# Kernel optimization log

Measured on AMD Instinct MI355X. Metric: run time of the kernel, lower is better.

Reference implementation:

```python
import jax, jax.numpy as jnp
import numpy as np
from jax import lax

SOBEL_X = np.array([[1, 0, -1], [2, 0, -2], [1, 0, -1]], dtype=np.float32)
SOBEL_Y = np.array([[1, 2, 1], [0, 0, 0], [-1, -2, -1]], dtype=np.float32)
K_XX = np.array([[1, -2, 1], [2, -4, 2], [1, -2, 1]], dtype=np.float32)
K_YY = np.array([[1, 2, 1], [-2, -4, -2], [1, 2, 1]], dtype=np.float32)
K_XY = np.array([[-1, 0, 1], [0, 0, 0], [1, 0, -1]], dtype=np.float32)
EPS = 1e-6


def _depthwise3x3(x, k2d):
    # x: [B, C, H, W]; k2d: [3, 3] -> depthwise conv, groups = C, padding 1
    C = x.shape[1]
    kernel = jnp.broadcast_to(jnp.asarray(k2d, dtype=x.dtype), (C, 1, 3, 3))
    return lax.conv_general_dilated(
        x, kernel, window_strides=(1, 1), padding=((1, 1), (1, 1)),
        dimension_numbers=("NCHW", "OIHW", "NCHW"), feature_group_count=C)


def setup_inputs() -> dict:
    key = jax.random.key(0)
    x = jax.random.normal(key, (16, 128, 128, 128), dtype=jnp.float32)
    return {"x": x}


def reference(x):
    Gx = _depthwise3x3(x, SOBEL_X)
    Gy = _depthwise3x3(x, SOBEL_Y)
    Ixx = _depthwise3x3(x, K_XX)
    Iyy = _depthwise3x3(x, K_YY)
    Ixy = _depthwise3x3(x, K_XY)

    Gx2 = Gx * Gx
    Gy2 = Gy * Gy
    grad_mag = jnp.sqrt(Gx2 + Gy2 + EPS)
    numerator = Gx2 * Iyy - 2.0 * Gx * Gy * Ixy + Gy2 * Ixx
    denominator = (Gx2 + Gy2 + EPS) ** 1.5
    curvature = numerator / denominator

    attn = jax.nn.softmax(grad_mag + curvature, axis=1) + 1.0  # softmax over channels
    return attn * x
```

## Files before the change

kernel.cpp:

```cpp
#include <hip/hip_runtime.h>


#define GCA_B 16
#define GCA_C 128
#define GCA_H 128
#define GCA_W 128
#define CGRP  16
#define CPW   (GCA_C/CGRP)

__device__ __forceinline__ float gca_score6(float cpl, float cpc, float cpr,
                                            float cml, float cmc, float cmr,
                                            float cyl, float cyc, float cyr) {
    const float Gx  = cpl - cpr;
    const float Gy  = fmaf(2.f, cmc, cml + cmr);
    const float Ixx = fmaf(-2.f, cpc, cpl + cpr);
    const float Ixy = cmr - cml;
    const float Iyy = fmaf(2.f, cyc, cyl + cyr);
    const float gy2 = Gy * Gy;
    const float g2e = fmaf(Gx, Gx, gy2 + 1e-6f);
    const float r   = rsqrtf(g2e);
    const float gm  = g2e * r;
    const float t   = Gx * Iyy;
    const float p   = Gy * Ixy;
    const float inner = fmaf(-2.f, p, t);
    const float q   = gy2 * Ixx;
    const float num = fmaf(Gx, inner, q);
    const float r3  = (r * r) * r;
    return fmaf(num, r3, gm);
}

__global__ __launch_bounds__(512) void gca_fused6(const float* __restrict__ x,
                                                  float* __restrict__ out) {
    const int tx = threadIdx.x;
    const int ty = threadIdx.y;

    const int id  = blockIdx.x;
    const int swz = ((id & 7) << 8) | (id >> 3);
    const int h   = swz & 127;
    const int b   = swz >> 7;

    const int w0 = tx * 4;
    const int c0 = ty * CPW;

    const int hm = (h > 0) ? h - 1 : 0;
    const int hp = (h < GCA_H - 1) ? h + 1 : GCA_H - 1;
    const float mh0 = (h > 0) ? 1.f : 0.f;
    const float mh2 = (h < GCA_H - 1) ? 1.f : 0.f;
    const float mwA = (tx > 0) ? 1.f : 0.f;
    const float mwB = (tx < 31) ? 1.f : 0.f;

    const size_t plane = (size_t)GCA_H * GCA_W;
    const float* base = x   + ((size_t)b * GCA_C + c0) * plane;
    float* obase      = out + ((size_t)b * GCA_C + c0) * plane;

    const int r0off = hm * GCA_W + w0;
    const int r1off = h  * GCA_W + w0;
    const int r2off = hp * GCA_W + w0;

    float4 s[CPW];
    float4 lmax = make_float4(-3.0e38f, -3.0e38f, -3.0e38f, -3.0e38f);

    #pragma unroll
    for (int i = 0; i < CPW; ++i) {
        const float* p = base + (size_t)i * plane;
        float4 v0 = *(const float4*)(p + r0off);
        const float4 v1 = *(const float4*)(p + r1off);
        float4 v2 = *(const float4*)(p + r2off);
        float L0 = __shfl_up(v0.w, 1), R0 = __shfl_down(v0.x, 1);
        const float L1 = __shfl_up(v1.w, 1), R1 = __shfl_down(v1.x, 1);
        float L2 = __shfl_up(v2.w, 1), R2 = __shfl_down(v2.x, 1);

        v0.x *= mh0; v0.y *= mh0; v0.z *= mh0; v0.w *= mh0; L0 *= mh0; R0 *= mh0;
        v2.x *= mh2; v2.y *= mh2; v2.z *= mh2; v2.w *= mh2; L2 *= mh2; R2 *= mh2;

        float cp0, cp1, cp2, cp3, cp4, cp5;
        float cm0, cm1, cm2, cm3, cm4, cm5;
        float cy0, cy1, cy2, cy3, cy4, cy5;

        cp0 = fmaf(2.f, L1, L0 + L2) * mwA;
        cm0 = (L0 - L2) * mwA;
        cy0 = fmaf(-4.f, L1 * mwA, cp0);

        cp1 = fmaf(2.f, v1.x, v0.x + v2.x); cm1 = v0.x - v2.x; cy1 = fmaf(-4.f, v1.x, cp1);
        cp2 = fmaf(2.f, v1.y, v0.y + v2.y); cm2 = v0.y - v2.y; cy2 = fmaf(-4.f, v1.y, cp2);
        cp3 = fmaf(2.f, v1.z, v0.z + v2.z); cm3 = v0.z - v2.z; cy3 = fmaf(-4.f, v1.z, cp3);
        cp4 = fmaf(2.f, v1.w, v0.w + v2.w); cm4 = v0.w - v2.w; cy4 = fmaf(-4.f, v1.w, cp4);

        cp5 = fmaf(2.f, R1, R0 + R2) * mwB;
        cm5 = (R0 - R2) * mwB;
        cy5 = fmaf(-4.f, R1 * mwB, cp5);

        float4 sc;
        sc.x = gca_score6(cp0, cp1, cp2,  cm0, cm1, cm2,  cy0, cy1, cy2);
        sc.y = gca_score6(cp1, cp2, cp3,  cm1, cm2, cm3,  cy1, cy2, cy3);
        sc.z = gca_score6(cp2, cp3, cp4,  cm2, cm3, cm4,  cy2, cy3, cy4);
        sc.w = gca_score6(cp3, cp4, cp5,  cm3, cm4, cm5,  cy3, cy4, cy5);
        s[i] = sc;
        lmax.x = fmaxf(lmax.x, sc.x);
        lmax.y = fmaxf(lmax.y, sc.y);
        lmax.z = fmaxf(lmax.z, sc.z);
        lmax.w = fmaxf(lmax.w, sc.w);
    }

    __shared__ float4 redmax[CGRP][32];
    __shared__ float4 redsum[CGRP][32];

    redmax[ty][tx] = lmax;
    __syncthreads();
    float4 gmax = make_float4(-3.0e38f, -3.0e38f, -3.0e38f, -3.0e38f);
    #pragma unroll
    for (int g = 0; g < CGRP; ++g) {
        const float4 m = redmax[g][tx];
        gmax.x = fmaxf(gmax.x, m.x);
        gmax.y = fmaxf(gmax.y, m.y);
        gmax.z = fmaxf(gmax.z, m.z);
        gmax.w = fmaxf(gmax.w, m.w);
    }

    float4 lsum = make_float4(0.f, 0.f, 0.f, 0.f);
    #pragma unroll
    for (int i = 0; i < CPW; ++i) {
        float4 e;
        e.x = __expf(s[i].x - gmax.x);
        e.y = __expf(s[i].y - gmax.y);
        e.z = __expf(s[i].z - gmax.z);
        e.w = __expf(s[i].w - gmax.w);
        s[i] = e;
        lsum.x += e.x; lsum.y += e.y; lsum.z += e.z; lsum.w += e.w;
    }
    redsum[ty][tx] = lsum;
    __syncthreads();
    float4 tot = make_float4(0.f, 0.f, 0.f, 0.f);
    #pragma unroll
    for (int g = 0; g < CGRP; ++g) {
        const float4 sm = redsum[g][tx];
        tot.x += sm.x; tot.y += sm.y; tot.z += sm.z; tot.w += sm.w;
    }
    const float invx = 1.f / tot.x, invy = 1.f / tot.y;
    const float invz = 1.f / tot.z, invw = 1.f / tot.w;

    #pragma unroll
    for (int i = 0; i < CPW; ++i) {
        const float4 xv = *(const float4*)(base + (size_t)i * plane + r1off);
        float4 o;
        o.x = fmaf(s[i].x * invx, xv.x, xv.x);
        o.y = fmaf(s[i].y * invy, xv.y, xv.y);
        o.z = fmaf(s[i].z * invz, xv.z, xv.z);
        o.w = fmaf(s[i].w * invw, xv.w, xv.w);
        *(float4*)(obase + (size_t)i * plane + r1off) = o;
    }
}

extern "C" void kernel_launch(void* const* d_in, const int* in_sizes, int n_in,
                              void* d_out, int out_size, void* d_ws, size_t ws_size,
                              hipStream_t stream) {
    (void)in_sizes; (void)n_in; (void)d_ws; (void)ws_size; (void)out_size;
    const float* x = (const float*)d_in[0];
    float* out = (float*)d_out;
    dim3 block(32, CGRP, 1);
    dim3 grid(GCA_B * GCA_H, 1, 1);
    gca_fused6<<<grid, block, 0, stream>>>(x, out);
}
```

Baseline: 69.90 us.

## Process two output rows per block to reuse vertical halo loads

Each block now computes two adjacent rows, loading four input rows instead of three per output row, so vertical-neighbour reads are shared between the two outputs. Horizontal neighbours are now obtained by shuffling the vertically combined column sums (six shuffles per row) rather than the raw row values. The grid is halved, and registers per thread roughly double (two score arrays), which may lower occupancy or cause spills under the 512-thread launch bound.

```diff
diff --git a/kernel.cpp b/kernel.cpp
--- a/kernel.cpp
+++ b/kernel.cpp
@@ -8,7 +8,7 @@
 #define CGRP  16
 #define CPW   (GCA_C/CGRP)
 
-__device__ __forceinline__ float gca_score6(float cpl, float cpc, float cpr,
+__device__ __forceinline__ float gca_score8(float cpl, float cpc, float cpr,
                                             float cml, float cmc, float cmr,
                                             float cyl, float cyc, float cyr) {
     const float Gx  = cpl - cpr;
@@ -29,23 +29,55 @@
     return fmaf(num, r3, gm);
 }
 
-__global__ __launch_bounds__(512) void gca_fused6(const float* __restrict__ x,
+#define GCA_ROW_SCORES(vA, vB, vC, scv, lmaxv)                                 \
+    {                                                                          \
+        const float cpA = fmaf(2.f, (vB).x, (vA).x + (vC).x);                  \
+        const float cmA = (vA).x - (vC).x;                                     \
+        const float cyA = fmaf(-4.f, (vB).x, cpA);                             \
+        const float cpB = fmaf(2.f, (vB).y, (vA).y + (vC).y);                  \
+        const float cmB = (vA).y - (vC).y;                                     \
+        const float cyB = fmaf(-4.f, (vB).y, cpB);                             \
+        const float cpC = fmaf(2.f, (vB).z, (vA).z + (vC).z);                  \
+        const float cmC = (vA).z - (vC).z;                                     \
+        const float cyC = fmaf(-4.f, (vB).z, cpC);                             \
+        const float cpD = fmaf(2.f, (vB).w, (vA).w + (vC).w);                  \
+        const float cmD = (vA).w - (vC).w;                                     \
+        const float cyD = fmaf(-4.f, (vB).w, cpD);                             \
+        const float cpL = __shfl_up(cpD, 1) * mwA;                             \
+        const float cmL = __shfl_up(cmD, 1) * mwA;                             \
+        const float cyL = __shfl_up(cyD, 1) * mwA;                             \
+        const float cpR = __shfl_down(cpA, 1) * mwB;                           \
+        const float cmR = __shfl_down(cmA, 1) * mwB;                           \
+        const float cyR = __shfl_down(cyA, 1) * mwB;                           \
+        (scv).x = gca_score8(cpL, cpA, cpB, cmL, cmA, cmB, cyL, cyA, cyB);     \
+        (scv).y = gca_score8(cpA, cpB, cpC, cmA, cmB, cmC, cyA, cyB, cyC);     \
+        (scv).z = gca_score8(cpB, cpC, cpD, cmB, cmC, cmD, cyB, cyC, cyD);     \
+        (scv).w = gca_score8(cpC, cpD, cpR, cmC, cmD, cmR, cyC, cyD, cyR);     \
+        (lmaxv).x = fmaxf((lmaxv).x, (scv).x);                                 \
+        (lmaxv).y = fmaxf((lmaxv).y, (scv).y);                                 \
+        (lmaxv).z = fmaxf((lmaxv).z, (scv).z);                                 \
+        (lmaxv).w = fmaxf((lmaxv).w, (scv).w);                                 \
+    }
+
+__global__ __launch_bounds__(512) void gca_fused8(const float* __restrict__ x,
                                                   float* __restrict__ out) {
     const int tx = threadIdx.x;
     const int ty = threadIdx.y;
 
     const int id  = blockIdx.x;
-    const int swz = ((id & 7) << 8) | (id >> 3);
-    const int h   = swz & 127;
-    const int b   = swz >> 7;
+    const int swz = ((id & 7) << 7) | (id >> 3);
+    const int hq  = swz & 63;
+    const int b   = swz >> 6;
+    const int h0  = hq * 2;
+    const int h1  = h0 + 1;
 
     const int w0 = tx * 4;
     const int c0 = ty * CPW;
 
-    const int hm = (h > 0) ? h - 1 : 0;
-    const int hp = (h < GCA_H - 1) ? h + 1 : GCA_H - 1;
-    const float mh0 = (h > 0) ? 1.f : 0.f;
-    const float mh2 = (h < GCA_H - 1) ? 1.f : 0.f;
+    const int hmm = (h0 > 0) ? h0 - 1 : 0;
+    const int hpp = (h1 < GCA_H - 1) ? h1 + 1 : GCA_H - 1;
+    const float mTop = (h0 > 0) ? 1.f : 0.f;
+    const float mBot = (h1 < GCA_H - 1) ? 1.f : 0.f;
     const float mwA = (tx > 0) ? 1.f : 0.f;
     const float mwB = (tx < 31) ? 1.f : 0.f;
 
@@ -53,101 +85,94 @@
     const float* base = x   + ((size_t)b * GCA_C + c0) * plane;
     float* obase      = out + ((size_t)b * GCA_C + c0) * plane;
 
-    const int r0off = hm * GCA_W + w0;
-    const int r1off = h  * GCA_W + w0;
-    const int r2off = hp * GCA_W + w0;
+    const int offm = hmm * GCA_W + w0;
+    const int off0 = h0  * GCA_W + w0;
+    const int off1 = h1  * GCA_W + w0;
+    const int offp = hpp * GCA_W + w0;
 
-    float4 s[CPW];
-    float4 lmax = make_float4(-3.0e38f, -3.0e38f, -3.0e38f, -3.0e38f);
+    float4 sT[CPW], sB[CPW];
+    float4 lmaxT = make_float4(-3.0e38f, -3.0e38f, -3.0e38f, -3.0e38f);
+    float4 lmaxB = lmaxT;
 
     #pragma unroll
     for (int i = 0; i < CPW; ++i) {
         const float* p = base + (size_t)i * plane;
-        float4 v0 = *(const float4*)(p + r0off);
-        const float4 v1 = *(const float4*)(p + r1off);
-        float4 v2 = *(const float4*)(p + r2off);
-        float L0 = __shfl_up(v0.w, 1), R0 = __shfl_down(v0.x, 1);
-        const float L1 = __shfl_up(v1.w, 1), R1 = __shfl_down(v1.x, 1);
-        float L2 = __shfl_up(v2.w, 1), R2 = __shfl_down(v2.x, 1);
+        float4 vm = *(const float4*)(p + offm);
+        const float4 v0 = *(const float4*)(p + off0);
+        const float4 v1 = *(const float4*)(p + off1);
+        float4 vp = *(const float4*)(p + offp);
+        vm.x *= mTop; vm.y *= mTop; vm.z *= mTop; vm.w *= mTop;
+        vp.x *= mBot; vp.y *= mBot; vp.z *= mBot; vp.w *= mBot;
 
-        v0.x *= mh0; v0.y *= mh0; v0.z *= mh0; v0.w *= mh0; L0 *= mh0; R0 *= mh0;
-        v2.x *= mh2; v2.y *= mh2; v2.z *= mh2; v2.w *= mh2; L2 *= mh2; R2 *= mh2;
-
-        float cp0, cp1, cp2, cp3, cp4, cp5;
-        float cm0, cm1, cm2, cm3, cm4, cm5;
-        float cy0, cy1, cy2, cy3, cy4, cy5;
-
-        cp0 = fmaf(2.f, L1, L0 + L2) * mwA;
-        cm0 = (L0 - L2) * mwA;
-        cy0 = fmaf(-4.f, L1 * mwA, cp0);
-
-        cp1 = fmaf(2.f, v1.x, v0.x + v2.x); cm1 = v0.x - v2.x; cy1 = fmaf(-4.f, v1.x, cp1);
-        cp2 = fmaf(2.f, v1.y, v0.y + v2.y); cm2 = v0.y - v2.y; cy2 = fmaf(-4.f, v1.y, cp2);
-        cp3 = fmaf(2.f, v1.z, v0.z + v2.z); cm3 = v0.z - v2.z; cy3 = fmaf(-4.f, v1.z, cp3);
-        cp4 = fmaf(2.f, v1.w, v0.w + v2.w); cm4 = v0.w - v2.w; cy4 = fmaf(-4.f, v1.w, cp4);
-
-        cp5 = fmaf(2.f, R1, R0 + R2) * mwB;
-        cm5 = (R0 - R2) * mwB;
-        cy5 = fmaf(-4.f, R1 * mwB, cp5);
-
-        float4 sc;
-        sc.x = gca_score6(cp0, cp1, cp2,  cm0, cm1, cm2,  cy0, cy1, cy2);
-        sc.y = gca_score6(cp1, cp2, cp3,  cm1, cm2, cm3,  cy1, cy2, cy3);
-        sc.z = gca_score6(cp2, cp3, cp4,  cm2, cm3, cm4,  cy2, cy3, cy4);
-        sc.w = gca_score6(cp3, cp4, cp5,  cm3, cm4, cm5,  cy3, cy4, cy5);
-        s[i] = sc;
-        lmax.x = fmaxf(lmax.x, sc.x);
-        lmax.y = fmaxf(lmax.y, sc.y);
-        lmax.z = fmaxf(lmax.z, sc.z);
-        lmax.w = fmaxf(lmax.w, sc.w);
+        GCA_ROW_SCORES(vm, v0, v1, sT[i], lmaxT);
+        GCA_ROW_SCORES(v0, v1, vp, sB[i], lmaxB);
     }
 
-    __shared__ float4 redmax[CGRP][32];
-    __shared__ float4 redsum[CGRP][32];
+    __shared__ float4 redmaxT[CGRP][32];
+    __shared__ float4 redmaxB[CGRP][32];
+    __shared__ float4 redsumT[CGRP][32];
+    __shared__ float4 redsumB[CGRP][32];
 
-    redmax[ty][tx] = lmax;
+    redmaxT[ty][tx] = lmaxT;
+    redmaxB[ty][tx] = lmaxB;
     __syncthreads();
-    float4 gmax = make_float4(-3.0e38f, -3.0e38f, -3.0e38f, -3.0e38f);
+    float4 gmaxT = make_float4(-3.0e38f, -3.0e38f, -3.0e38f, -3.0e38f);
+    float4 gmaxB = gmaxT;
     #pragma unroll
     for (int g = 0; g < CGRP; ++g) {
-        const float4 m = redmax[g][tx];
-        gmax.x = fmaxf(gmax.x, m.x);
-        gmax.y = fmaxf(gmax.y, m.y);
-        gmax.z = fmaxf(gmax.z, m.z);
-        gmax.w = fmaxf(gmax.w, m.w);
+        const float4 mt = redmaxT[g][tx];
+        const float4 mb = redmaxB[g][tx];
+        gmaxT.x = fmaxf(gmaxT.x, mt.x); gmaxT.y = fmaxf(gmaxT.y, mt.y);
+        gmaxT.z = fmaxf(gmaxT.z, mt.z); gmaxT.w = fmaxf(gmaxT.w, mt.w);
+        gmaxB.x = fmaxf(gmaxB.x, mb.x); gmaxB.y = fmaxf(gmaxB.y, mb.y);
+        gmaxB.z = fmaxf(gmaxB.z, mb.z); gmaxB.w = fmaxf(gmaxB.w, mb.w);
     }
 
-    float4 lsum = make_float4(0.f, 0.f, 0.f, 0.f);
+    float4 lsumT = make_float4(0.f, 0.f, 0.f, 0.f);
+    float4 lsumB = lsumT;
     #pragma unroll
     for (int i = 0; i < CPW; ++i) {
-        float4 e;
-        e.x = __expf(s[i].x - gmax.x);
-        e.y = __expf(s[i].y - gmax.y);
-        e.z = __expf(s[i].z - gmax.z);
-        e.w = __expf(s[i].w - gmax.w);
-        s[i] = e;
-        lsum.x += e.x; lsum.y += e.y; lsum.z += e.z; lsum.w += e.w;
+        float4 eT, eB;
+        eT.x = __expf(sT[i].x - gmaxT.x); eT.y = __expf(sT[i].y - gmaxT.y);
+        eT.z = __expf(sT[i].z - gmaxT.z); eT.w = __expf(sT[i].w - gmaxT.w);
+        eB.x = __expf(sB[i].x - gmaxB.x); eB.y = __expf(sB[i].y - gmaxB.y);
+        eB.z = __expf(sB[i].z - gmaxB.z); eB.w = __expf(sB[i].w - gmaxB.w);
+        sT[i] = eT; sB[i] = eB;
+        lsumT.x += eT.x; lsumT.y += eT.y; lsumT.z += eT.z; lsumT.w += eT.w;
+        lsumB.x += eB.x; lsumB.y += eB.y; lsumB.z += eB.z; lsumB.w += eB.w;
     }
-    redsum[ty][tx] = lsum;
+    redsumT[ty][tx] = lsumT;
+    redsumB[ty][tx] = lsumB;
     __syncthreads();
-    float4 tot = make_float4(0.f, 0.f, 0.f, 0.f);
+    float4 totT = make_float4(0.f, 0.f, 0.f, 0.f);
+    float4 totB = totT;
     #pragma unroll
     for (int g = 0; g < CGRP; ++g) {
-        const float4 sm = redsum[g][tx];
-        tot.x += sm.x; tot.y += sm.y; tot.z += sm.z; tot.w += sm.w;
+        const float4 st = redsumT[g][tx];
+        const float4 sb = redsumB[g][tx];
+        totT.x += st.x; totT.y += st.y; totT.z += st.z; totT.w += st.w;
+        totB.x += sb.x; totB.y += sb.y; totB.z += sb.z; totB.w += sb.w;
     }
-    const float invx = 1.f / tot.x, invy = 1.f / tot.y;
-    const float invz = 1.f / tot.z, invw = 1.f / tot.w;
+    const float invTx = 1.f / totT.x, invTy = 1.f / totT.y;
+    const float invTz = 1.f / totT.z, invTw = 1.f / totT.w;
+    const float invBx = 1.f / totB.x, invBy = 1.f / totB.y;
+    const float invBz = 1.f / totB.z, invBw = 1.f / totB.w;
 
     #pragma unroll
     for (int i = 0; i < CPW; ++i) {
-        const float4 xv = *(const float4*)(base + (size_t)i * plane + r1off);
-        float4 o;
-        o.x = fmaf(s[i].x * invx, xv.x, xv.x);
-        o.y = fmaf(s[i].y * invy, xv.y, xv.y);
-        o.z = fmaf(s[i].z * invz, xv.z, xv.z);
-        o.w = fmaf(s[i].w * invw, xv.w, xv.w);
-        *(float4*)(obase + (size_t)i * plane + r1off) = o;
+        const float4 xT = *(const float4*)(base + (size_t)i * plane + off0);
+        const float4 xB = *(const float4*)(base + (size_t)i * plane + off1);
+        float4 oT, oB;
+        oT.x = fmaf(sT[i].x * invTx, xT.x, xT.x);
+        oT.y = fmaf(sT[i].y * invTy, xT.y, xT.y);
+        oT.z = fmaf(sT[i].z * invTz, xT.z, xT.z);
+        oT.w = fmaf(sT[i].w * invTw, xT.w, xT.w);
+        oB.x = fmaf(sB[i].x * invBx, xB.x, xB.x);
+        oB.y = fmaf(sB[i].y * invBy, xB.y, xB.y);
+        oB.z = fmaf(sB[i].z * invBz, xB.z, xB.z);
+        oB.w = fmaf(sB[i].w * invBw, xB.w, xB.w);
+        *(float4*)(obase + (size_t)i * plane + off0) = oT;
+        *(float4*)(obase + (size_t)i * plane + off1) = oB;
     }
 }
 
@@ -158,6 +183,6 @@
     const float* x = (const float*)d_in[0];
     float* out = (float*)d_out;
     dim3 block(32, CGRP, 1);
-    dim3 grid(GCA_B * GCA_H, 1, 1);
-    gca_fused6<<<grid, block, 0, stream>>>(x, out);
+    dim3 grid(GCA_B * GCA_H / 2, 1, 1);
+    gca_fused8<<<grid, block, 0, stream>>>(x, out);
 }
```

Result: slower. 75.21 us (+7.6%).
